# Performance work log

Hardware: AMD Instinct MI355X
Metric: run time of the kernel (lower is better)

## Reference

```python
import jax, jax.numpy as jnp
import numpy as np

EPS = 1e-5

def _layer_norm(x, w, b):
    mu = jnp.mean(x, axis=-1, keepdims=True)
    var = jnp.mean(jnp.square(x - mu), axis=-1, keepdims=True)
    return (x - mu) * jax.lax.rsqrt(var + EPS) * w + b

def setup_inputs() -> dict:
    key = jax.random.key(0)
    ks = jax.random.split(key, 5)
    B, S, C = 1, 512, 128
    scale = 1.0 / np.sqrt(C)
    return {
        "z_ij": jax.random.normal(ks[0], (B, S, S, C), dtype=jnp.float32),
        "ln_w": jnp.ones((C,), jnp.float32),
        "ln_b": jnp.zeros((C,), jnp.float32),
        "wa": jax.random.normal(ks[1], (C, C), dtype=jnp.float32) * scale,
        "wb": jax.random.normal(ks[2], (C, C), dtype=jnp.float32) * scale,
        "wg": jax.random.normal(ks[3], (C, C), dtype=jnp.float32) * scale,
        "fln_w": jnp.ones((C,), jnp.float32),
        "fln_b": jnp.zeros((C,), jnp.float32),
        "wf": jax.random.normal(ks[4], (C, C), dtype=jnp.float32) * scale,
    }

def reference(z_ij, ln_w, ln_b, wa, wb, wg, fln_w, fln_b, wf):
    # z_ij: (B, S, S, C). torch Linear(x) == x @ W.T
    z = _layer_norm(z_ij, ln_w, ln_b)
    a = jax.nn.sigmoid(z @ wa.T)  # (B, S, S, C)
    b = jax.nn.sigmoid(z @ wb.T)
    g = jax.nn.sigmoid(z @ wg.T)
    # torch: einsum('...kic,...kjc->...ijc', a.transpose(-3,-2), b)
    # == out[i,j,c] = sum_k a[i,k,c] * b[k,j,c]
    p = jnp.einsum('bikc,bkjc->bijc', a, b)
    return g * (_layer_norm(p, fln_w, fln_b) @ wf.T)
```

## Files before the change

kernel.cpp:

```cpp
#include <hip/hip_runtime.h>

#define SS 512
#define CC 128
#define RR (SS*SS)

typedef unsigned short u16;
typedef unsigned int   u32;
typedef __attribute__((ext_vector_type(4))) float f32x4;
typedef __attribute__((ext_vector_type(8))) short s16x8;
typedef __attribute__((ext_vector_type(4))) u32   u32x4;

__device__ __forceinline__ float bf2f(u16 u){ u32 x = ((u32)u)<<16; float f; __builtin_memcpy(&f,&x,4); return f; }
__device__ __forceinline__ float sigf(float x){ return 1.f/(1.f + __expf(-x)); }

__device__ __forceinline__ u32 cvtpk(float lo, float hi){
  u32 r; asm("v_cvt_pk_bf16_f32 %0, %1, %2" : "=v"(r) : "v"(lo), "v"(hi)); return r;
}

typedef __attribute__((address_space(1))) void* gptr_t;
typedef __attribute__((address_space(3))) void* lptr_t;
__device__ __forceinline__ void load_lds16(const void* g, void* l){
  __builtin_amdgcn_global_load_lds((gptr_t)(g), (lptr_t)(l), 16, 0, 0);
}

__global__ void k0(const float* __restrict__ wa, const float* __restrict__ wb,
                   const float* __restrict__ wg, const float* __restrict__ wf,
                   u16* __restrict__ wabg, u16* __restrict__ wfbg)
{
  int t = blockIdx.x*256 + threadIdx.x;
  const float* srcs[4] = {wa, wb, wg, wf};
  int m = t >> 11;
  int e = (t & 2047) * 8;
  const float* s = srcs[m] + e;
  u32 pk[4];
  #pragma unroll
  for (int v=0; v<2; v++){
    f32x4 x = *reinterpret_cast<const f32x4*>(s + v*4);
    pk[v*2]   = cvtpk(x[0], x[1]);
    pk[v*2+1] = cvtpk(x[2], x[3]);
  }
  u16* dst = (m==3) ? (wfbg + e) : (wabg + m*16384 + e);
  *reinterpret_cast<u32x4*>(dst) = *reinterpret_cast<u32x4*>(pk);
}

__global__ __launch_bounds__(256,6) void k1(
    const float* __restrict__ z, const float* __restrict__ lnw, const float* __restrict__ lnb,
    const u16* __restrict__ wabg,
    u16* __restrict__ a_t, u16* __restrict__ b_t, u16* __restrict__ g_out,
    float* __restrict__ SaPart)
{
  __shared__ __align__(16) u16 un[9216];
  __shared__ __align__(16) u16 wk[32*128];
  u16 (*zn)[136] = reinterpret_cast<u16(*)[136]>(un);
  u16* tr = un;
  const int tid = threadIdx.x;
  const int r0  = blockIdx.x * 64;
  const int lane = tid & 63, w = tid >> 6;
  const int iI   = r0 >> 9;
  const int kblk = (r0 >> 6) & 7;

  auto stageW = [&](int m, int qt){
    const u16* Wb = wabg + m*16384 + qt*4096;
    #pragma unroll
    for (int s=0;s<2;s++){
      int lr = s*16 + (tid>>4);
      const u16* gsrc = Wb + lr*128 + (((tid&15) ^ (lr&7))<<3);
      load_lds16((const void*)gsrc, (void*)&wk[s*2048 + w*512]);
    }
  };

  stageW(0,0);

  {
    int row = tid >> 2, q = tid & 3;
    const float* src = z + (size_t)(r0+row)*CC + q*32;
    float v[32]; float s = 0.f, s2 = 0.f;
    #pragma unroll
    for (int i=0;i<8;i++){
      f32x4 t = *reinterpret_cast<const f32x4*>(src + i*4);
      #pragma unroll
      for (int e=0;e<4;e++){ float x = t[e]; v[i*4+e]=x; s += x; s2 += x*x; }
    }
    s  += __shfl_xor(s,1);  s2 += __shfl_xor(s2,1);
    s  += __shfl_xor(s,2);  s2 += __shfl_xor(s2,2);
    float mu  = s * (1.f/128.f);
    float var = s2*(1.f/128.f) - mu*mu;
    float rs  = rsqrtf(var + 1e-5f);
    #pragma unroll
    for (int i=0;i<4;i++){
      u32 pk[4];
      #pragma unroll
      for (int e=0;e<8;e+=2){
        int ci = i*8+e; int c = q*32 + ci;
        float y0 = (v[ci]  -mu)*rs*lnw[c]   + lnb[c];
        float y1 = (v[ci+1]-mu)*rs*lnw[c+1] + lnb[c+1];
        pk[e>>1] = cvtpk(y0, y1);
      }
      *reinterpret_cast<u32x4*>(&zn[row][q*32 + i*8]) = *reinterpret_cast<u32x4*>(pk);
    }
  }
  __syncthreads();

  s16x8 af[4];
  #pragma unroll
  for (int ks=0;ks<4;ks++)
    af[ks] = *reinterpret_cast<const s16x8*>(&zn[w*16 + (lane&15)][ks*32 + (lane>>4)*8]);

  for (int m=0;m<3;m++){
    f32x4 acc[8];
    #pragma unroll
    for (int cb=0;cb<8;cb++) acc[cb] = (f32x4){0.f,0.f,0.f,0.f};

    for (int qt=0; qt<4; ++qt){
      __syncthreads();
      #pragma unroll
      for (int cc=0; cc<2; ++cc){
        int cb = qt*2 + cc;
        int lr = cc*16 + (lane&15);
        const int rx = (lr&7)<<3;
        const u16* base = &wk[lr*128];
        s16x8 b0 = *reinterpret_cast<const s16x8*>(&base[(  0 + (lane>>4)*8) ^ rx]);
        s16x8 b1 = *reinterpret_cast<const s16x8*>(&base[( 32 + (lane>>4)*8) ^ rx]);
        s16x8 b2 = *reinterpret_cast<const s16x8*>(&base[( 64 + (lane>>4)*8) ^ rx]);
        s16x8 b3 = *reinterpret_cast<const s16x8*>(&base[( 96 + (lane>>4)*8) ^ rx]);
        acc[cb] = __builtin_amdgcn_mfma_f32_16x16x32_bf16(af[0], b0, acc[cb], 0,0,0);
        acc[cb] = __builtin_amdgcn_mfma_f32_16x16x32_bf16(af[1], b1, acc[cb], 0,0,0);
        acc[cb] = __builtin_amdgcn_mfma_f32_16x16x32_bf16(af[2], b2, acc[cb], 0,0,0);
        acc[cb] = __builtin_amdgcn_mfma_f32_16x16x32_bf16(af[3], b3, acc[cb], 0,0,0);
      }
      __syncthreads();
      if (qt<3) stageW(m, qt+1);
    }

    if (m < 2){
      #pragma unroll
      for (int cb=0;cb<8;cb++){
        int col = cb*16 + (lane&15);
        int rbase = w*16 + (lane>>4)*4;
        u32 p0 = cvtpk(sigf(acc[cb][0])-0.5f, sigf(acc[cb][1])-0.5f);
        u32 p1 = cvtpk(sigf(acc[cb][2])-0.5f, sigf(acc[cb][3])-0.5f);
        u32* d = reinterpret_cast<u32*>(&tr[col*72 + rbase]);
        d[0] = p0; d[1] = p1;
      }
      __syncthreads();
      stageW(m+1, 0);
      {
        int c = tid>>1, half = tid&1;
        u16* dst = (m==0 ? a_t : b_t) + ((size_t)c<<18) + r0 + half*32;
        const u16* srcl = &tr[c*72 + half*32];
        float s = 0.f;
        #pragma unroll
        for (int e=0;e<4;e++){
          u32x4 t = *reinterpret_cast<const u32x4*>(srcl + e*8);
          *reinterpret_cast<u32x4*>(dst + e*8) = t;
          #pragma unroll
          for (int q=0;q<4;q++){ u32 v = t[q]; s += bf2f((u16)v) + bf2f((u16)(v>>16)); }
        }
        if (m==0){
          s += __shfl_xor(s, 1);
          if ((tid&1)==0) SaPart[(kblk<<16) + (iI<<7) + c] = s;
        }
      }
      __syncthreads();
    } else {
      u16* gb = &tr[0];
      #pragma unroll
      for (int cb=0;cb<8;cb++){
        int col = cb*16 + (lane&15);
        int rbase = w*16 + (lane>>4)*4;
        #pragma unroll
        for (int q=0;q<4;q++){
          float sg = sigf(acc[cb][q]);
          gb[(rbase+q)*136 + col] = (u16)cvtpk(sg, sg);
        }
      }
      __syncthreads();
      {
        int row = tid>>2, qo = tid&3;
        u16* dst = g_out + (size_t)(r0+row)*CC + qo*32;
        const u16* srcl = &gb[row*136 + qo*32];
        #pragma unroll
        for (int e=0;e<4;e++)
          *reinterpret_cast<u32x4*>(dst + e*8) = *reinterpret_cast<const u32x4*>(srcl + e*8);
      }
    }
  }
}

__global__ __launch_bounds__(256,8) void k1b(const u16* __restrict__ b_t, u16* __restrict__ bT,
                                             float* __restrict__ SbPart)
{
  __shared__ __align__(16) u16 tile[64][72];
  const int tid = threadIdx.x;
  const int c  = blockIdx.x >> 6;
  const int t  = blockIdx.x & 63;
  const int k0 = (t>>3)*64, j0 = (t&7)*64;
  const u16* src = b_t + ((size_t)c<<18);
  {
    int row = tid>>3, chunk = tid&7;
    #pragma unroll
    for (int pass=0; pass<2; pass++){
      int k = row + pass*32;
      const u16* s = src + (size_t)(k0+k)*SS + j0 + chunk*8;
      u32x4 v = *reinterpret_cast<const u32x4*>(s);
      int cs = chunk ^ ((k>>3)&7);
      *reinterpret_cast<u32x4*>(&tile[k][cs*8]) = v;
    }
  }
  __syncthreads();
  {
    int j = tid>>2, part = tid&3;
    u32 pk[8];
    float sb = 0.f;
    #pragma unroll
    for (int i=0;i<16;i+=2){
      int ka = part*16 + i;
      int key = (ka>>3)&7;
      u16 va = tile[ka  ][(((j>>3)^key)*8) + (j&7)];
      u16 vb = tile[ka+1][(((j>>3)^key)*8) + (j&7)];
      pk[i>>1] = (u32)va | ((u32)vb<<16);
      sb += bf2f(va) + bf2f(vb);
    }
    u16* dst = bT + ((size_t)c<<18) + (size_t)(j0+j)*SS + k0 + part*16;
    *reinterpret_cast<u32x4*>(dst)   = *reinterpret_cast<u32x4*>(pk);
    *reinterpret_cast<u32x4*>(dst+8) = *reinterpret_cast<u32x4*>(pk+4);
    sb += __shfl_xor(sb, 1);
    sb += __shfl_xor(sb, 2);
    if (part==0) SbPart[(((c<<9) + j0 + j)<<3) + (k0>>6)] = sb;
  }
}

__global__ void k1c(const float* __restrict__ SaPart, const float* __restrict__ SbPart,
                    float* __restrict__ Sa, float* __restrict__ Sb)
{
  int idx = blockIdx.x*256 + threadIdx.x;
  if (idx < 65536){
    int i = idx >> 7, c = idx & 127;
    float s = 0.f;
    #pragma unroll
    for (int b=0;b<8;b++) s += SaPart[(b<<16) + (i<<7) + c];
    Sa[(c<<9) + i] = s;
  } else {
    int cj = idx & 65535;
    const float* src = SbPart + ((size_t)cj << 3);
    float s = 0.f;
    #pragma unroll
    for (int b=0;b<8;b++) s += src[b];
    Sb[cj] = s;
  }
}

__global__ __launch_bounds__(256,3) void k2(const u16* __restrict__ a_t, const u16* __restrict__ bT,
                                            const float* __restrict__ Sa, const float* __restrict__ Sb,
                                            _Float16* __restrict__ ph)
{
  __shared__ __align__(16) u16 As[2][128*64];
  __shared__ __align__(16) u16 Bs[128*64];
  const int tid = threadIdx.x;
  const int lane = tid & 63, w = tid >> 6;
  const int bid = blockIdx.x;
  const int swz = (bid & 7) * 256 + (bid >> 3);
  const int c   = swz >> 4;
  const int t16 = swz & 15;
  const int i0 = (t16 >> 2) * 128, j0 = (t16 & 3) * 128;
  const u16* Ag = a_t + ((size_t)c<<18);
  const u16* Bg = bT  + ((size_t)c<<18);
  const int pr = lane>>3, slot = lane&7;

  auto stageA = [&](int kt, int buf){
    #pragma unroll
    for (int s=0;s<4;s++){
      int rbase = w*32 + s*8;
      int rl = rbase + pr;
      const u16* g = Ag + (size_t)(i0+rl)*SS + kt*64 + ((slot^pr)*8);
      load_lds16((const void*)g, (void*)&As[buf][rbase*64]);
    }
  };
  auto stageB = [&](int kt){
    #pragma unroll
    for (int s=0;s<4;s++){
      int rbase = w*32 + s*8;
      int rl = rbase + pr;
      const u16* g = Bg + (size_t)(j0+rl)*SS + kt*64 + ((slot^pr)*8);
      load_lds16((const void*)g, (void*)&Bs[rbase*64]);
    }
  };

  f32x4 acc[4][4];
  #pragma unroll
  for (int a=0;a<4;a++)
    #pragma unroll
    for (int b=0;b<4;b++) acc[a][b] = (f32x4){0.f,0.f,0.f,0.f};
  const int wr = w>>1, wc = w&1;

  stageA(0, 0);
  for (int kt=0; kt<8; ++kt){
    stageB(kt);
    if (kt < 7){
      stageA(kt+1, (kt+1)&1);
      asm volatile("s_waitcnt vmcnt(4)" ::: "memory");
    } else {
      asm volatile("s_waitcnt vmcnt(0)" ::: "memory");
    }
    __builtin_amdgcn_s_barrier();
    const u16* Ab = &As[kt&1][0];
    #pragma unroll
    for (int ks=0;ks<2;ks++){
      s16x8 af[4], bfv[4];
      #pragma unroll
      for (int f=0; f<4; f++){
        int i = wr*64 + f*16 + (lane&15);
        int ch = (ks*4 + (lane>>4)) ^ (i&7);
        af[f] = *reinterpret_cast<const s16x8*>(&Ab[i*64 + ch*8]);
        int j = wc*64 + f*16 + (lane&15);
        int chb = (ks*4 + (lane>>4)) ^ (j&7);
        bfv[f] = *reinterpret_cast<const s16x8*>(&Bs[j*64 + chb*8]);
      }
      #pragma unroll
      for (int fi=0;fi<4;fi++)
        #pragma unroll
        for (int fj=0;fj<4;fj++)
          acc[fi][fj] = __builtin_amdgcn_mfma_f32_16x16x32_bf16(af[fi], bfv[fj], acc[fi][fj], 0,0,0);
    }
    asm volatile("s_waitcnt lgkmcnt(0)" ::: "memory");
    __builtin_amdgcn_s_barrier();
  }

  _Float16* P = ph + ((size_t)c<<18);
  const float* SaC = Sa + (c<<9);
  const float* SbC = Sb + (c<<9);
  float sbv[4];
  #pragma unroll
  for (int fj=0;fj<4;fj++) sbv[fj] = SbC[j0 + wc*64 + fj*16 + (lane&15)];
  #pragma unroll
  for (int fi=0;fi<4;fi++){
    int rbase = i0 + wr*64 + fi*16 + (lane>>4)*4;
    #pragma unroll
    for (int q=0;q<4;q++){
      float sav = SaC[rbase+q];
      #pragma unroll
      for (int fj=0;fj<4;fj++){
        int col = j0 + wc*64 + fj*16 + (lane&15);
        P[(size_t)(rbase+q)*SS + col] = (_Float16)(0.5f*(sav + sbv[fj]) + acc[fi][fj][q]);
      }
    }
  }
}

__global__ __launch_bounds__(256,4) void k3(const _Float16* __restrict__ ph, const u16* __restrict__ g,
    const float* __restrict__ flnw, const float* __restrict__ flnb,
    const u16* __restrict__ wfbg, float* __restrict__ out)
{
  __shared__ __align__(16) u16 znp[64][136];
  __shared__ __align__(16) u16 wk[64*128];
  __shared__ __align__(16) float red[4][64];
  __shared__ __align__(16) float muv[64], rsv[64];
  const int tid = threadIdx.x;
  const int rr0 = blockIdx.x * 64;
  const int lane = tid&63, w = tid>>6;
  const int pos = tid & 63, cq = tid >> 6;

  auto stageWF = [&](int h){
    const u16* Wb = wfbg + h*8192;
    #pragma unroll
    for (int s=0;s<4;s++){
      int lr = s*16 + (tid>>4);
      const u16* gsrc = Wb + lr*128 + (((tid&15) ^ (lr&7))<<3);
      load_lds16((const void*)gsrc, (void*)&wk[s*2048 + w*512]);
    }
  };

  stageWF(0);

  float pv[32];
  {
    const _Float16* src = ph + rr0 + pos;
    float s = 0.f;
    #pragma unroll
    for (int ci=0;ci<32;ci++){
      int c = cq*32 + ci;
      float x = (float)src[((size_t)c)<<18];
      pv[ci] = x; s += x;
    }
    red[cq][pos] = s;
  }
  __syncthreads();
  if (tid < 64) muv[tid] = (red[0][tid]+red[1][tid]+red[2][tid]+red[3][tid]) * (1.f/128.f);
  __syncthreads();
  float mu = muv[pos];
  {
    float s2 = 0.f;
    #pragma unroll
    for (int ci=0;ci<32;ci++){ float d = pv[ci]-mu; s2 += d*d; }
    red[cq][pos] = s2;
  }
  __syncthreads();
  if (tid < 64) rsv[tid] = rsqrtf((red[0][tid]+red[1][tid]+red[2][tid]+red[3][tid])*(1.f/128.f) + 1e-5f);
  __syncthreads();
  float rs = rsv[pos];
  {
    u32 pk[4];
    #pragma unroll
    for (int ii=0;ii<4;ii++){
      #pragma unroll
      for (int e=0;e<8;e+=2){
        int ci = ii*8+e; int c = cq*32+ci;
        float y0 = (pv[ci]  -mu)*rs*flnw[c]   + flnb[c];
        float y1 = (pv[ci+1]-mu)*rs*flnw[c+1] + flnb[c+1];
        pk[e>>1] = cvtpk(y0, y1);
      }
      *reinterpret_cast<u32x4*>(&znp[pos][cq*32 + ii*8]) = *reinterpret_cast<u32x4*>(pk);
    }
  }
  __syncthreads();

  f32x4 acc[8];
  #pragma unroll
  for (int cb=0;cb<8;cb++) acc[cb] = (f32x4){0.f,0.f,0.f,0.f};

  #pragma unroll
  for (int ks=0;ks<4;ks++){
    s16x8 af = *reinterpret_cast<const s16x8*>(&znp[w*16 + (lane&15)][ks*32 + (lane>>4)*8]);
    #pragma unroll
    for (int cb=0;cb<4;cb++){
      int lr = cb*16 + (lane&15);
      const int rx = (lr&7)<<3;
      s16x8 bf = *reinterpret_cast<const s16x8*>(&wk[lr*128 + ((ks*32 + (lane>>4)*8) ^ rx)]);
      acc[cb] = __builtin_amdgcn_mfma_f32_16x16x32_bf16(af, bf, acc[cb], 0,0,0);
    }
  }
  __syncthreads();
  stageWF(1);
  __syncthreads();

  #pragma unroll
  for (int ks=0;ks<4;ks++){
    s16x8 af = *reinterpret_cast<const s16x8*>(&znp[w*16 + (lane&15)][ks*32 + (lane>>4)*8]);
    #pragma unroll
    for (int cb=4;cb<8;cb++){
      int lr = (cb-4)*16 + (lane&15);
      const int rx = (lr&7)<<3;
      s16x8 bf = *reinterpret_cast<const s16x8*>(&wk[lr*128 + ((ks*32 + (lane>>4)*8) ^ rx)]);
      acc[cb] = __builtin_amdgcn_mfma_f32_16x16x32_bf16(af, bf, acc[cb], 0,0,0);
    }
  }
  __syncthreads();

  u16* gb = &znp[0][0];
  {
    int row = tid>>2, qo = tid&3;
    const u16* src = g + (size_t)(rr0+row)*CC + qo*32;
    #pragma unroll
    for (int e=0;e<4;e++)
      *reinterpret_cast<u32x4*>(&gb[row*136 + qo*32 + e*8]) = *reinterpret_cast<const u32x4*>(src + e*8);
  }
  __syncthreads();
  #pragma unroll
  for (int cb=0;cb<8;cb++){
    int col = cb*16 + (lane&15);
    int rbase = w*16 + (lane>>4)*4;
    #pragma unroll
    for (int q=0;q<4;q++){
      float gv = bf2f(gb[(rbase+q)*136 + col]);
      out[(size_t)(rr0+rbase+q)*CC + col] = gv * acc[cb][q];
    }
  }
}

extern "C" void kernel_launch(void* const* d_in, const int* in_sizes, int n_in,
                              void* d_out, int out_size, void* d_ws, size_t ws_size,
                              hipStream_t stream)
{
  const float* z    = (const float*)d_in[0];
  const float* lnw  = (const float*)d_in[1];
  const float* lnb  = (const float*)d_in[2];
  const float* wa   = (const float*)d_in[3];
  const float* wb   = (const float*)d_in[4];
  const float* wg   = (const float*)d_in[5];
  const float* flnw = (const float*)d_in[6];
  const float* flnb = (const float*)d_in[7];
  const float* wf   = (const float*)d_in[8];
  float* out = (float*)d_out;

  char* ws = (char*)d_ws;
  u16* a_t = (u16*)(ws);
  u16* bT  = (u16*)(ws + ((size_t)64<<20));
  u16* g   = (u16*)(ws + ((size_t)128<<20));
  _Float16* ph = (_Float16*)(ws + ((size_t)192<<20));
  u16* b_t = (u16*)(ws + ((size_t)192<<20));
  u16* wfbg = (u16*)(ws + ((size_t)256<<20));

  char* ob = (char*)d_out;
  u16*   wabg   = (u16*)ob;
  float* SaPart = (float*)(ob + ((size_t)1<<20));
  float* SbPart = (float*)(ob + ((size_t)3<<20));
  float* Sa     = (float*)(ob + ((size_t)5<<20));
  float* Sb     = (float*)(ob + ((size_t)5<<20) + ((size_t)256<<10));

  k0 <<<32,   256, 0, stream>>>(wa, wb, wg, wf, wabg, wfbg);
  k1 <<<4096, 256, 0, stream>>>(z, lnw, lnb, wabg, a_t, b_t, g, SaPart);
  k1b<<<8192, 256, 0, stream>>>(b_t, bT, SbPart);
  k1c<<<512,  256, 0, stream>>>(SaPart, SbPart, Sa, Sb);
  k2 <<<2048, 256, 0, stream>>>(a_t, bT, Sa, Sb, ph);
  k3 <<<4096, 256, 0, stream>>>(ph, g, flnw, flnb, wfbg, out);
}
```

Baseline: 296.4 us.

## Recompute gate projection in final kernel instead of storing g

Moves the sigmoid gate projection out of the first projection kernel and into the final output kernel. The final kernel now re-reads z, redoes its layer norm and computes g with MFMA, so the bf16 g tensor is never written to or read back from memory. The cost is an extra read of the fp32 z input (twice the bytes of the bf16 g round-trip it replaces), more LDS and registers in k3 with lower launch bounds, and a second layer norm of z.

```diff
diff --git a/kernel.cpp b/kernel.cpp
--- a/kernel.cpp
+++ b/kernel.cpp
@@ -25,7 +25,7 @@
 
 __global__ void k0(const float* __restrict__ wa, const float* __restrict__ wb,
                    const float* __restrict__ wg, const float* __restrict__ wf,
-                   u16* __restrict__ wabg, u16* __restrict__ wfbg)
+                   u16* __restrict__ wabg, u16* __restrict__ wgbg, u16* __restrict__ wfbg)
 {
   int t = blockIdx.x*256 + threadIdx.x;
   const float* srcs[4] = {wa, wb, wg, wf};
@@ -39,14 +39,14 @@
     pk[v*2]   = cvtpk(x[0], x[1]);
     pk[v*2+1] = cvtpk(x[2], x[3]);
   }
-  u16* dst = (m==3) ? (wfbg + e) : (wabg + m*16384 + e);
+  u16* dst = (m<=1) ? (wabg + m*16384 + e) : (m==2 ? (wgbg + e) : (wfbg + e));
   *reinterpret_cast<u32x4*>(dst) = *reinterpret_cast<u32x4*>(pk);
 }
 
-__global__ __launch_bounds__(256,6) void k1(
+__global__ __launch_bounds__(256,4) void k1(
     const float* __restrict__ z, const float* __restrict__ lnw, const float* __restrict__ lnb,
     const u16* __restrict__ wabg,
-    u16* __restrict__ a_t, u16* __restrict__ b_t, u16* __restrict__ g_out,
+    u16* __restrict__ a_t, u16* __restrict__ b_t,
     float* __restrict__ SaPart)
 {
   __shared__ __align__(16) u16 un[9216];
@@ -106,11 +106,12 @@
   for (int ks=0;ks<4;ks++)
     af[ks] = *reinterpret_cast<const s16x8*>(&zn[w*16 + (lane&15)][ks*32 + (lane>>4)*8]);
 
-  for (int m=0;m<3;m++){
+  for (int m=0;m<2;m++){
     f32x4 acc[8];
     #pragma unroll
     for (int cb=0;cb<8;cb++) acc[cb] = (f32x4){0.f,0.f,0.f,0.f};
 
+    #pragma unroll
     for (int qt=0; qt<4; ++qt){
       __syncthreads();
       #pragma unroll
@@ -132,7 +133,9 @@
       if (qt<3) stageW(m, qt+1);
     }
 
-    if (m < 2){
+    if (m==0) stageW(1, 0);
+
+    {
       #pragma unroll
       for (int cb=0;cb<8;cb++){
         int col = cb*16 + (lane&15);
@@ -143,7 +146,6 @@
         d[0] = p0; d[1] = p1;
       }
       __syncthreads();
-      stageW(m+1, 0);
       {
         int c = tid>>1, half = tid&1;
         u16* dst = (m==0 ? a_t : b_t) + ((size_t)c<<18) + r0 + half*32;
@@ -153,36 +155,17 @@
         for (int e=0;e<4;e++){
           u32x4 t = *reinterpret_cast<const u32x4*>(srcl + e*8);
           *reinterpret_cast<u32x4*>(dst + e*8) = t;
-          #pragma unroll
-          for (int q=0;q<4;q++){ u32 v = t[q]; s += bf2f((u16)v) + bf2f((u16)(v>>16)); }
+          if (m==0){
+            #pragma unroll
+            for (int q=0;q<4;q++){ u32 v = t[q]; s += bf2f((u16)v) + bf2f((u16)(v>>16)); }
+          }
         }
         if (m==0){
           s += __shfl_xor(s, 1);
           if ((tid&1)==0) SaPart[(kblk<<16) + (iI<<7) + c] = s;
         }
       }
-      __syncthreads();
-    } else {
-      u16* gb = &tr[0];
-      #pragma unroll
-      for (int cb=0;cb<8;cb++){
-        int col = cb*16 + (lane&15);
-        int rbase = w*16 + (lane>>4)*4;
-        #pragma unroll
-        for (int q=0;q<4;q++){
-          float sg = sigf(acc[cb][q]);
-          gb[(rbase+q)*136 + col] = (u16)cvtpk(sg, sg);
-        }
-      }
-      __syncthreads();
-      {
-        int row = tid>>2, qo = tid&3;
-        u16* dst = g_out + (size_t)(r0+row)*CC + qo*32;
-        const u16* srcl = &gb[row*136 + qo*32];
-        #pragma unroll
-        for (int e=0;e<4;e++)
-          *reinterpret_cast<u32x4*>(dst + e*8) = *reinterpret_cast<const u32x4*>(srcl + e*8);
-      }
+      if (m==0) __syncthreads();
     }
   }
 }
@@ -347,21 +330,26 @@
   }
 }
 
-__global__ __launch_bounds__(256,4) void k3(const _Float16* __restrict__ ph, const u16* __restrict__ g,
+__global__ __launch_bounds__(256,3) void k3(
+    const float* __restrict__ z, const float* __restrict__ lnw, const float* __restrict__ lnb,
+    const _Float16* __restrict__ ph,
     const float* __restrict__ flnw, const float* __restrict__ flnb,
-    const u16* __restrict__ wfbg, float* __restrict__ out)
-{
-  __shared__ __align__(16) u16 znp[64][136];
+    const u16* __restrict__ wgbg, const u16* __restrict__ wfbg,
+    float* __restrict__ out)
+{
+  __shared__ __align__(16) u16 un[8704];
+  __shared__ __align__(16) u16 gb[9216];
   __shared__ __align__(16) u16 wk[64*128];
   __shared__ __align__(16) float red[4][64];
   __shared__ __align__(16) float muv[64], rsv[64];
+  u16 (*zn)[136] = reinterpret_cast<u16(*)[136]>(un);
   const int tid = threadIdx.x;
   const int rr0 = blockIdx.x * 64;
   const int lane = tid&63, w = tid>>6;
   const int pos = tid & 63, cq = tid >> 6;
 
-  auto stageWF = [&](int h){
-    const u16* Wb = wfbg + h*8192;
+  auto stageWH = [&](const u16* Wsrc, int h){
+    const u16* Wb = Wsrc + h*8192;
     #pragma unroll
     for (int s=0;s<4;s++){
       int lr = s*16 + (tid>>4);
@@ -370,8 +358,93 @@
     }
   };
 
-  stageWF(0);
-
+  stageWH(wgbg, 0);
+
+  {
+    int row = tid >> 2, q = tid & 3;
+    const float* src = z + (size_t)(rr0+row)*CC + q*32;
+    float v[32]; float s = 0.f, s2 = 0.f;
+    #pragma unroll
+    for (int i=0;i<8;i++){
+      f32x4 t = *reinterpret_cast<const f32x4*>(src + i*4);
+      #pragma unroll
+      for (int e=0;e<4;e++){ float x = t[e]; v[i*4+e]=x; s += x; s2 += x*x; }
+    }
+    s  += __shfl_xor(s,1);  s2 += __shfl_xor(s2,1);
+    s  += __shfl_xor(s,2);  s2 += __shfl_xor(s2,2);
+    float mu  = s * (1.f/128.f);
+    float var = s2*(1.f/128.f) - mu*mu;
+    float rs  = rsqrtf(var + 1e-5f);
+    #pragma unroll
+    for (int i=0;i<4;i++){
+      u32 pk[4];
+      #pragma unroll
+      for (int e=0;e<8;e+=2){
+        int ci = i*8+e; int c = q*32 + ci;
+        float y0 = (v[ci]  -mu)*rs*lnw[c]   + lnb[c];
+        float y1 = (v[ci+1]-mu)*rs*lnw[c+1] + lnb[c+1];
+        pk[e>>1] = cvtpk(y0, y1);
+      }
+      *reinterpret_cast<u32x4*>(&zn[row][q*32 + i*8]) = *reinterpret_cast<u32x4*>(pk);
+    }
+  }
+  __syncthreads();
+
+  s16x8 afz[4];
+  #pragma unroll
+  for (int ks=0;ks<4;ks++)
+    afz[ks] = *reinterpret_cast<const s16x8*>(&zn[w*16 + (lane&15)][ks*32 + (lane>>4)*8]);
+
+  f32x4 accg[8];
+  #pragma unroll
+  for (int cb=0;cb<8;cb++) accg[cb] = (f32x4){0.f,0.f,0.f,0.f};
+
+  #pragma unroll
+  for (int cb=0;cb<4;cb++){
+    int lr = cb*16 + (lane&15);
+    const int rx = (lr&7)<<3;
+    const u16* base = &wk[lr*128];
+    s16x8 b0 = *reinterpret_cast<const s16x8*>(&base[(  0 + (lane>>4)*8) ^ rx]);
+    s16x8 b1 = *reinterpret_cast<const s16x8*>(&base[( 32 + (lane>>4)*8) ^ rx]);
+    s16x8 b2 = *reinterpret_cast<const s16x8*>(&base[( 64 + (lane>>4)*8) ^ rx]);
+    s16x8 b3 = *reinterpret_cast<const s16x8*>(&base[( 96 + (lane>>4)*8) ^ rx]);
+    accg[cb] = __builtin_amdgcn_mfma_f32_16x16x32_bf16(afz[0], b0, accg[cb], 0,0,0);
+    accg[cb] = __builtin_amdgcn_mfma_f32_16x16x32_bf16(afz[1], b1, accg[cb], 0,0,0);
+    accg[cb] = __builtin_amdgcn_mfma_f32_16x16x32_bf16(afz[2], b2, accg[cb], 0,0,0);
+    accg[cb] = __builtin_amdgcn_mfma_f32_16x16x32_bf16(afz[3], b3, accg[cb], 0,0,0);
+  }
+  __syncthreads();
+  stageWH(wgbg, 1);
+  __syncthreads();
+  #pragma unroll
+  for (int cb=4;cb<8;cb++){
+    int lr = (cb-4)*16 + (lane&15);
+    const int rx = (lr&7)<<3;
+    const u16* base = &wk[lr*128];
+    s16x8 b0 = *reinterpret_cast<const s16x8*>(&base[(  0 + (lane>>4)*8) ^ rx]);
+    s16x8 b1 = *reinterpret_cast<const s16x8*>(&base[( 32 + (lane>>4)*8) ^ rx]);
+    s16x8 b2 = *reinterpret_cast<const s16x8*>(&base[( 64 + (lane>>4)*8) ^ rx]);
+    s16x8 b3 = *reinterpret_cast<const s16x8*>(&base[( 96 + (lane>>4)*8) ^ rx]);
+    accg[cb] = __builtin_amdgcn_mfma_f32_16x16x32_bf16(afz[0], b0, accg[cb], 0,0,0);
+    accg[cb] = __builtin_amdgcn_mfma_f32_16x16x32_bf16(afz[1], b1, accg[cb], 0,0,0);
+    accg[cb] = __builtin_amdgcn_mfma_f32_16x16x32_bf16(afz[2], b2, accg[cb], 0,0,0);
+    accg[cb] = __builtin_amdgcn_mfma_f32_16x16x32_bf16(afz[3], b3, accg[cb], 0,0,0);
+  }
+  __syncthreads();
+
+  stageWH(wfbg, 0);
+
+  #pragma unroll
+  for (int cb=0;cb<8;cb++){
+    int col = cb*16 + (lane&15);
+    int rbase = w*16 + (lane>>4)*4;
+    u32 p0 = cvtpk(sigf(accg[cb][0]), sigf(accg[cb][1]));
+    u32 p1 = cvtpk(sigf(accg[cb][2]), sigf(accg[cb][3]));
+    u32* d = reinterpret_cast<u32*>(&gb[col*72 + rbase]);
+    d[0] = p0; d[1] = p1;
+  }
+
+  u16 (*znp)[136] = reinterpret_cast<u16(*)[136]>(un);
   float pv[32];
   {
     const _Float16* src = ph + rr0 + pos;
@@ -417,7 +490,6 @@
   f32x4 acc[8];
   #pragma unroll
   for (int cb=0;cb<8;cb++) acc[cb] = (f32x4){0.f,0.f,0.f,0.f};
-
   #pragma unroll
   for (int ks=0;ks<4;ks++){
     s16x8 af = *reinterpret_cast<const s16x8*>(&znp[w*16 + (lane&15)][ks*32 + (lane>>4)*8]);
@@ -430,9 +502,8 @@
     }
   }
   __syncthreads();
-  stageWF(1);
-  __syncthreads();
-
+  stageWH(wfbg, 1);
+  __syncthreads();
   #pragma unroll
   for (int ks=0;ks<4;ks++){
     s16x8 af = *reinterpret_cast<const s16x8*>(&znp[w*16 + (lane&15)][ks*32 + (lane>>4)*8]);
@@ -444,24 +515,14 @@
       acc[cb] = __builtin_amdgcn_mfma_f32_16x16x32_bf16(af, bf, acc[cb], 0,0,0);
     }
   }
-  __syncthreads();
-
-  u16* gb = &znp[0][0];
-  {
-    int row = tid>>2, qo = tid&3;
-    const u16* src = g + (size_t)(rr0+row)*CC + qo*32;
-    #pragma unroll
-    for (int e=0;e<4;e++)
-      *reinterpret_cast<u32x4*>(&gb[row*136 + qo*32 + e*8]) = *reinterpret_cast<const u32x4*>(src + e*8);
-  }
-  __syncthreads();
+
   #pragma unroll
   for (int cb=0;cb<8;cb++){
     int col = cb*16 + (lane&15);
     int rbase = w*16 + (lane>>4)*4;
     #pragma unroll
     for (int q=0;q<4;q++){
-      float gv = bf2f(gb[(rbase+q)*136 + col]);
+      float gv = bf2f(gb[col*72 + rbase + q]);
       out[(size_t)(rr0+rbase+q)*CC + col] = gv * acc[cb][q];
     }
   }
@@ -485,10 +546,10 @@
   char* ws = (char*)d_ws;
   u16* a_t = (u16*)(ws);
   u16* bT  = (u16*)(ws + ((size_t)64<<20));
-  u16* g   = (u16*)(ws + ((size_t)128<<20));
   _Float16* ph = (_Float16*)(ws + ((size_t)192<<20));
   u16* b_t = (u16*)(ws + ((size_t)192<<20));
-  u16* wfbg = (u16*)(ws + ((size_t)256<<20));
+  u16* wgbg = (u16*)(ws + ((size_t)256<<20));
+  u16* wfbg = wgbg + 16384;
 
   char* ob = (char*)d_out;
   u16*   wabg   = (u16*)ob;
@@ -497,10 +558,10 @@
   float* Sa     = (float*)(ob + ((size_t)5<<20));
   float* Sb     = (float*)(ob + ((size_t)5<<20) + ((size_t)256<<10));
 
-  k0 <<<32,   256, 0, stream>>>(wa, wb, wg, wf, wabg, wfbg);
-  k1 <<<4096, 256, 0, stream>>>(z, lnw, lnb, wabg, a_t, b_t, g, SaPart);
+  k0 <<<32,   256, 0, stream>>>(wa, wb, wg, wf, wabg, wgbg, wfbg);
+  k1 <<<4096, 256, 0, stream>>>(z, lnw, lnb, wabg, a_t, b_t, SaPart);
   k1b<<<8192, 256, 0, stream>>>(b_t, bT, SbPart);
   k1c<<<512,  256, 0, stream>>>(SaPart, SbPart, Sa, Sb);
   k2 <<<2048, 256, 0, stream>>>(a_t, bT, Sa, Sb, ph);
-  k3 <<<4096, 256, 0, stream>>>(ph, g, flnw, flnb, wfbg, out);
-}
+  k3 <<<4096, 256, 0, stream>>>(z, lnw, lnb, ph, flnw, flnb, wgbg, wfbg, out);
+}
```

New measurement: 285.7 us. 3.6% less time.
